# Optimization experiments

Measured on AMD Instinct MI355X. Metric: run time of the kernel, lower is better.

Reference implementation:

```python
import jax, jax.numpy as jnp
import numpy as np

DX = 1.0      # grid spacing
RHO = 1.0     # density
NU = 0.1      # viscosity
DT = 0.1      # timestep
STEPS = 1000  # Jacobi relaxation iterations

# Periodic (CIRCULAR) finite-difference stencils via jnp.roll on the last two axes.

def ddx(f):
    # central difference along x (axis -2)
    return (jnp.roll(f, -1, axis=-2) - jnp.roll(f, 1, axis=-2)) / (2.0 * DX)

def ddy(f):
    # central difference along y (axis -1)
    return (jnp.roll(f, -1, axis=-1) - jnp.roll(f, 1, axis=-1)) / (2.0 * DX)

def neighbor_sum(f):
    # 4-neighbor sum: LapInv stencil used by the Jacobi step
    return (jnp.roll(f, 1, axis=-2) + jnp.roll(f, -1, axis=-2)
            + jnp.roll(f, 1, axis=-1) + jnp.roll(f, -1, axis=-1))

def laplacian(f):
    # 5-point Laplacian / dx^2
    return (neighbor_sum(f) - 4.0 * f) / (DX * DX)


def setup_inputs() -> dict:
    key = jax.random.key(0)
    k1, k2 = jax.random.split(key)
    X = jax.random.normal(k1, (2, 1, 512, 512), dtype=jnp.float32)
    forcing = jax.random.normal(k2, (2, 1, 512, 512), dtype=jnp.float32)
    t = jnp.zeros((), dtype=jnp.float32)
    return {"t": t, "X": X, "forcing": forcing}


def reference(t, X, forcing):
    # advection (v . grad) v : X[0]*dXi/dx + X[1]*dXi/dy, broadcast over vector dim
    adv = X[0] * ddx(X) + X[1] * ddy(X)              # (2, C, H, W)
    partial = -adv + NU * laplacian(X) + forcing      # (2, C, H, W)
    # divergence of partial -> pressure Poisson RHS
    B = RHO * (ddx(partial[0]) + ddy(partial[1])) / DT  # (C, H, W)

    def poisson_jacobi_step(phi, _):
        phi = (neighbor_sum(phi) - B * (DX * DX)) / 4.0
        return phi, None

    phi, _ = jax.lax.scan(poisson_jacobi_step, B, xs=None, length=STEPS)
    grad_phi = jnp.stack([ddx(phi), ddy(phi)])        # (2, C, H, W)
    return partial - grad_phi / RHO
```

## Files before the change

kernel.cpp:

```cpp
#include <hip/hip_runtime.h>
#include <math.h>


#define HH 512
#define WW 512
#define NCELL (HH * WW)
#define NU_C 0.1f
#define PI_F 3.14159265358979323846f
#define PADDED 576

__device__ __forceinline__ int padi(int i) { return i + (i >> 3); }

__device__ __forceinline__ float2 cadd(float2 a, float2 b) { return make_float2(a.x + b.x, a.y + b.y); }
__device__ __forceinline__ float2 csub(float2 a, float2 b) { return make_float2(a.x - b.x, a.y - b.y); }
__device__ __forceinline__ float2 cmul(float2 a, float2 b) {
    return make_float2(a.x * b.x - a.y * b.y, a.x * b.y + a.y * b.x);
}

template <int S>
__device__ __forceinline__ float2 cmul_tw(float2 a, float2 w) {
    float wy = (S < 0) ? w.y : -w.y;
    return make_float2(a.x * w.x - a.y * wy, a.x * wy + a.y * w.x);
}

template <int S>
__device__ __forceinline__ void bfly8(float2 r[8]) {
    const float c = 0.70710678118654752f;
    const float s = (float)S;
    float2 e0 = cadd(r[0], r[4]), f0 = csub(r[0], r[4]);
    float2 e1 = cadd(r[2], r[6]), f1 = csub(r[2], r[6]);
    float2 g0 = cadd(r[1], r[5]), h0 = csub(r[1], r[5]);
    float2 g1 = cadd(r[3], r[7]), h1 = csub(r[3], r[7]);
    float2 E0 = cadd(e0, e1), E2 = csub(e0, e1);
    float2 if1 = make_float2(-s * f1.y, s * f1.x);
    float2 E1 = cadd(f0, if1), E3 = csub(f0, if1);
    float2 O0 = cadd(g0, g1), O2 = csub(g0, g1);
    float2 ih1 = make_float2(-s * h1.y, s * h1.x);
    float2 O1 = cadd(h0, ih1), O3 = csub(h0, ih1);
    float2 t1 = make_float2(c * (O1.x - s * O1.y), c * (O1.y + s * O1.x));
    float2 t2 = make_float2(-s * O2.y, s * O2.x);
    float2 t3 = make_float2(-c * (O3.x + s * O3.y), -c * (O3.y - s * O3.x));
    r[0] = cadd(E0, O0); r[4] = csub(E0, O0);
    r[1] = cadd(E1, t1); r[5] = csub(E1, t1);
    r[2] = cadd(E2, t2); r[6] = csub(E2, t2);
    r[3] = cadd(E3, t3); r[7] = csub(E3, t3);
}

struct Twid { float2 s1[8]; float2 s2[8]; };

__device__ __forceinline__ void make_tw(Twid& tw, int t) {
    float sn, cs;
    sincosf(-2.0f * PI_F * (float)(t & 7) * (1.0f / 64.0f), &sn, &cs);
    float2 T1 = make_float2(cs, sn);
    tw.s1[0] = make_float2(1.0f, 0.0f);
#pragma unroll
    for (int m = 1; m < 8; ++m) tw.s1[m] = cmul(tw.s1[m - 1], T1);
    sincosf(-2.0f * PI_F * (float)t * (1.0f / 512.0f), &sn, &cs);
    float2 T2 = make_float2(cs, sn);
    tw.s2[0] = make_float2(1.0f, 0.0f);
#pragma unroll
    for (int m = 1; m < 8; ++m) tw.s2[m] = cmul(tw.s2[m - 1], T2);
}

template <int S>
__device__ __forceinline__ void fft512(float2 r[8], const Twid& tw,
                                       float2* b0, float2* b1, int t) {
    bfly8<S>(r);
#pragma unroll
    for (int k = 0; k < 8; ++k) b0[padi(8 * t + k)] = r[k];
    __syncthreads();
#pragma unroll
    for (int m = 0; m < 8; ++m) r[m] = b0[padi(t + 64 * m)];
#pragma unroll
    for (int m = 1; m < 8; ++m) r[m] = cmul_tw<S>(r[m], tw.s1[m]);
    bfly8<S>(r);
    int base = ((t >> 3) << 6) + (t & 7);
#pragma unroll
    for (int k = 0; k < 8; ++k) b1[padi(base + 8 * k)] = r[k];
    __syncthreads();
#pragma unroll
    for (int m = 0; m < 8; ++m) r[m] = b1[padi(t + 64 * m)];
#pragma unroll
    for (int m = 1; m < 8; ++m) r[m] = cmul_tw<S>(r[m], tw.s2[m]);
    bfly8<S>(r);
}

__global__ __launch_bounds__(64) void kA(const float* __restrict__ X,
                                         const float* __restrict__ F,
                                         float* __restrict__ p,
                                         float2* __restrict__ Zt) {
    __shared__ float2 b0[PADDED], b1[PADDED];
    int i = blockIdx.x, t = threadIdx.x;
    Twid tw; make_tw(tw, t);
    int ip = (i + 1) & 511, im = (i + 511) & 511;
    const float* X0 = X;
    const float* X1 = X + NCELL;
    float2 r[8];
#pragma unroll
    for (int m = 0; m < 8; ++m) {
        int j = t + 64 * m;
        int jp = (j + 1) & 511, jm = (j + 511) & 511;
        float x0c = X0[i * WW + j], x1c = X1[i * WW + j];
        float aip = X0[ip * WW + j], aim = X0[im * WW + j];
        float ajp = X0[i * WW + jp], ajm = X0[i * WW + jm];
        float p0 = -(x0c * (aip - aim) * 0.5f + x1c * (ajp - ajm) * 0.5f)
                 + NU_C * (aip + aim + ajp + ajm - 4.0f * x0c) + F[i * WW + j];
        float bip = X1[ip * WW + j], bim = X1[im * WW + j];
        float bjp = X1[i * WW + jp], bjm = X1[i * WW + jm];
        float p1 = -(x0c * (bip - bim) * 0.5f + x1c * (bjp - bjm) * 0.5f)
                 + NU_C * (bip + bim + bjp + bjm - 4.0f * x1c) + F[NCELL + i * WW + j];
        p[i * WW + j] = p0;
        p[NCELL + i * WW + j] = p1;
        r[m] = make_float2(p0, p1);
    }
    fft512<-1>(r, tw, b0, b1, t);
#pragma unroll
    for (int k = 0; k < 8; ++k) Zt[i * 512 + t + 64 * k] = r[k];
}

__global__ __launch_bounds__(128) void kB(const float2* __restrict__ Zt,
                                          float2* __restrict__ W1) {
    __shared__ float2 b0[2][PADDED], b1[2][PADDED];
    const int b = blockIdx.x;
    const int w = threadIdx.x >> 6, t = threadIdx.x & 63;
    const int cw = (b == 0) ? (w ? 256 : 0) : (w ? 512 - b : b);
    const int mw = (b == 0) ? w : (w ^ 1);
    Twid tw; make_tw(tw, t);
    float2 r[8];
#pragma unroll
    for (int m = 0; m < 8; ++m) r[m] = Zt[(t + 64 * m) * 512 + cw];
    fft512<-1>(r, tw, b0[w], b1[w], t);
#pragma unroll
    for (int k = 0; k < 8; ++k) b0[w][t + 64 * k] = r[k];
    __syncthreads();

    float shy, chy;
    sincosf(PI_F * (float)cw * (1.0f / 512.0f), &shy, &chy);
    float sy = 2.0f * shy * chy;
    float qy = shy * shy;
    float sh, ch;
    sincosf(PI_F * (float)t * (1.0f / 512.0f), &sh, &ch);
    const float c8 = 0.92387953251128675613f;
    const float s8 = 0.38268343236508977173f;
#pragma unroll
    for (int k = 0; k < 8; ++k) {
        int ki = t + 64 * k;
        int mi = (HH - ki) & 511;
        float2 z  = r[k];
        float2 zc = b0[mw][mi];
        float sx = 2.0f * sh * ch;
        float qx = sh * sh;
        float qs = qx + qy;
        float beta = 0.0f;
        if (ki != 0 || cw != 0) {
            float rN;
            if (qs < 1.0f)      rN = expf(1000.0f * log1pf(-qs));
            else if (qs > 1.0f) rN = expf(1000.0f * logf(qs - 1.0f));
            else                rN = 0.0f;
            float M = rN - (1.0f - rN) / (4.0f * qs);
            beta = -10.0f * M * (1.0f / (512.0f * 512.0f));
        }
        float su  = sx * sx + sy * sy;
        float u2x = sx * sx - sy * sy;
        float u2y = 2.0f * sx * sy;
        float cx = zc.x, cy = -zc.y;
        float tx = u2x * cx - u2y * cy;
        float ty = u2x * cy + u2y * cx;
        float bh = 0.5f * beta;
        r[k] = make_float2(bh * (su * z.x + tx), bh * (su * z.y + ty));
        float nch = ch * c8 - sh * s8;
        sh = sh * c8 + ch * s8;
        ch = nch;
    }
    __syncthreads();
    fft512<1>(r, tw, b0[w], b1[w], t);
#pragma unroll
    for (int k = 0; k < 8; ++k) W1[cw * 512 + t + 64 * k] = r[k];
}

__global__ __launch_bounds__(64) void kC(const float2* __restrict__ W1,
                                         const float* __restrict__ p,
                                         float* __restrict__ out) {
    __shared__ float2 b0[PADDED], b1[PADDED];
    int i = blockIdx.x, t = threadIdx.x;
    Twid tw; make_tw(tw, t);
    float pp0[8], pp1[8];
#pragma unroll
    for (int k = 0; k < 8; ++k) {
        pp0[k] = p[i * WW + t + 64 * k];
        pp1[k] = p[NCELL + i * WW + t + 64 * k];
    }
    float2 r[8];
#pragma unroll
    for (int m = 0; m < 8; ++m) r[m] = W1[(t + 64 * m) * 512 + i];
    fft512<1>(r, tw, b0, b1, t);
#pragma unroll
    for (int k = 0; k < 8; ++k) {
        int j = t + 64 * k;
        out[i * WW + j]         = pp0[k] - r[k].x;
        out[NCELL + i * WW + j] = pp1[k] - r[k].y;
    }
}

extern "C" void kernel_launch(void* const* d_in, const int* in_sizes, int n_in,
                              void* d_out, int out_size, void* d_ws, size_t ws_size,
                              hipStream_t stream) {
    const float* X = (const float*)d_in[1];
    const float* F = (const float*)d_in[2];
    float* out = (float*)d_out;
    float* ws  = (float*)d_ws;

    float*  p  = ws;
    float2* Zt = (float2*)(ws + 2 * NCELL);
    float2* W1 = Zt + NCELL;

    kA<<<dim3(512), dim3(64),  0, stream>>>(X, F, p, Zt);
    kB<<<dim3(256), dim3(128), 0, stream>>>(Zt, W1);
    kC<<<dim3(512), dim3(64),  0, stream>>>(W1, p, out);
}
```

Before: 78.79 us.

## Recompute stencil in final kernel instead of storing intermediate, remap block indices

Removes the intermediate 'partial' buffer. kA no longer writes it and kC recomputes the advection/diffusion stencil from X and F instead of reading it back. Block-to-row and block-to-column mappings are also permuted, likely to spread strided column accesses across memory channels or cache slices. This trades about 2 MB of write plus read traffic for extra stencil loads and arithmetic in kC.

```diff
diff --git a/kernel.cpp b/kernel.cpp
--- a/kernel.cpp
+++ b/kernel.cpp
@@ -85,17 +85,12 @@
     bfly8<S>(r);
 }
 
-__global__ __launch_bounds__(64) void kA(const float* __restrict__ X,
-                                         const float* __restrict__ F,
-                                         float* __restrict__ p,
-                                         float2* __restrict__ Zt) {
-    __shared__ float2 b0[PADDED], b1[PADDED];
-    int i = blockIdx.x, t = threadIdx.x;
-    Twid tw; make_tw(tw, t);
-    int ip = (i + 1) & 511, im = (i + 511) & 511;
+__device__ __forceinline__ void stencil_row(const float* __restrict__ X,
+                                            const float* __restrict__ F,
+                                            int i, int t, float p0r[8], float p1r[8]) {
+    const int ip = (i + 1) & 511, im = (i + 511) & 511;
     const float* X0 = X;
     const float* X1 = X + NCELL;
-    float2 r[8];
 #pragma unroll
     for (int m = 0; m < 8; ++m) {
         int j = t + 64 * m;
@@ -103,16 +98,27 @@
         float x0c = X0[i * WW + j], x1c = X1[i * WW + j];
         float aip = X0[ip * WW + j], aim = X0[im * WW + j];
         float ajp = X0[i * WW + jp], ajm = X0[i * WW + jm];
-        float p0 = -(x0c * (aip - aim) * 0.5f + x1c * (ajp - ajm) * 0.5f)
-                 + NU_C * (aip + aim + ajp + ajm - 4.0f * x0c) + F[i * WW + j];
+        p0r[m] = -(x0c * (aip - aim) * 0.5f + x1c * (ajp - ajm) * 0.5f)
+               + NU_C * (aip + aim + ajp + ajm - 4.0f * x0c) + F[i * WW + j];
         float bip = X1[ip * WW + j], bim = X1[im * WW + j];
         float bjp = X1[i * WW + jp], bjm = X1[i * WW + jm];
-        float p1 = -(x0c * (bip - bim) * 0.5f + x1c * (bjp - bjm) * 0.5f)
-                 + NU_C * (bip + bim + bjp + bjm - 4.0f * x1c) + F[NCELL + i * WW + j];
-        p[i * WW + j] = p0;
-        p[NCELL + i * WW + j] = p1;
-        r[m] = make_float2(p0, p1);
+        p1r[m] = -(x0c * (bip - bim) * 0.5f + x1c * (bjp - bjm) * 0.5f)
+               + NU_C * (bip + bim + bjp + bjm - 4.0f * x1c) + F[NCELL + i * WW + j];
     }
+}
+
+__global__ __launch_bounds__(64) void kA(const float* __restrict__ X,
+                                         const float* __restrict__ F,
+                                         float2* __restrict__ Zt) {
+    __shared__ float2 b0[PADDED], b1[PADDED];
+    const int b = blockIdx.x, t = threadIdx.x;
+    const int i = (b & 7) * 64 + (b >> 3);
+    Twid tw; make_tw(tw, t);
+    float p0r[8], p1r[8];
+    stencil_row(X, F, i, t, p0r, p1r);
+    float2 r[8];
+#pragma unroll
+    for (int m = 0; m < 8; ++m) r[m] = make_float2(p0r[m], p1r[m]);
     fft512<-1>(r, tw, b0, b1, t);
 #pragma unroll
     for (int k = 0; k < 8; ++k) Zt[i * 512 + t + 64 * k] = r[k];
@@ -123,8 +129,9 @@
     __shared__ float2 b0[2][PADDED], b1[2][PADDED];
     const int b = blockIdx.x;
     const int w = threadIdx.x >> 6, t = threadIdx.x & 63;
-    const int cw = (b == 0) ? (w ? 256 : 0) : (w ? 512 - b : b);
-    const int mw = (b == 0) ? w : (w ^ 1);
+    const int c0 = (b & 7) * 32 + (b >> 3);
+    const int cw = (c0 == 0) ? (w ? 256 : 0) : (w ? 512 - c0 : c0);
+    const int mw = (c0 == 0) ? w : (w ^ 1);
     Twid tw; make_tw(tw, t);
     float2 r[8];
 #pragma unroll
@@ -179,26 +186,24 @@
 }
 
 __global__ __launch_bounds__(64) void kC(const float2* __restrict__ W1,
-                                         const float* __restrict__ p,
+                                         const float* __restrict__ X,
+                                         const float* __restrict__ F,
                                          float* __restrict__ out) {
     __shared__ float2 b0[PADDED], b1[PADDED];
-    int i = blockIdx.x, t = threadIdx.x;
+    const int b = blockIdx.x, t = threadIdx.x;
+    const int i = (b & 7) * 64 + (b >> 3);
     Twid tw; make_tw(tw, t);
-    float pp0[8], pp1[8];
-#pragma unroll
-    for (int k = 0; k < 8; ++k) {
-        pp0[k] = p[i * WW + t + 64 * k];
-        pp1[k] = p[NCELL + i * WW + t + 64 * k];
-    }
     float2 r[8];
 #pragma unroll
     for (int m = 0; m < 8; ++m) r[m] = W1[(t + 64 * m) * 512 + i];
+    float p0r[8], p1r[8];
+    stencil_row(X, F, i, t, p0r, p1r);
     fft512<1>(r, tw, b0, b1, t);
 #pragma unroll
     for (int k = 0; k < 8; ++k) {
         int j = t + 64 * k;
-        out[i * WW + j]         = pp0[k] - r[k].x;
-        out[NCELL + i * WW + j] = pp1[k] - r[k].y;
+        out[i * WW + j]         = p0r[k] - r[k].x;
+        out[NCELL + i * WW + j] = p1r[k] - r[k].y;
     }
 }
 
@@ -210,11 +215,10 @@
     float* out = (float*)d_out;
     float* ws  = (float*)d_ws;
 
-    float*  p  = ws;
-    float2* Zt = (float2*)(ws + 2 * NCELL);
+    float2* Zt = (float2*)ws;
     float2* W1 = Zt + NCELL;
 
-    kA<<<dim3(512), dim3(64),  0, stream>>>(X, F, p, Zt);
+    kA<<<dim3(512), dim3(64),  0, stream>>>(X, F, Zt);
     kB<<<dim3(256), dim3(128), 0, stream>>>(Zt, W1);
-    kC<<<dim3(512), dim3(64),  0, stream>>>(W1, p, out);
-}
+    kC<<<dim3(512), dim3(64),  0, stream>>>(W1, X, F, out);
+}
```

Result: faster. 75.04 us (-4.8%).
